# Optimization experiments

Measured on AMD Instinct MI355X. Metric: run time of the kernel, lower is better.

Reference implementation:

```python
import jax, jax.numpy as jnp
import numpy as np

F_DIM, HID, H, DQ, DV = 1024, 4096, 16, 64, 64
EPS = 1e-6

def layer_norm(x, w, b):
    mu = jnp.mean(x, axis=-1, keepdims=True)
    var = jnp.mean(jnp.square(x - mu), axis=-1, keepdims=True)
    return (x - mu) * jax.lax.rsqrt(var + EPS) * w + b

def setup_inputs() -> dict:
    key = jax.random.key(0)
    ks = jax.random.split(key, 8)
    s = 0.02
    return {
        'x': jax.random.normal(ks[0], (4, 2048, F_DIM), dtype=jnp.float32),
        'ln1_w': jnp.ones((F_DIM,), jnp.float32),
        'ln1_b': jnp.zeros((F_DIM,), jnp.float32),
        'wq_w': jax.random.normal(ks[1], (H * DQ, F_DIM), jnp.float32) * s,
        'wq_b': jnp.zeros((H * DQ,), jnp.float32),
        'wk_w': jax.random.normal(ks[2], (H * DQ, F_DIM), jnp.float32) * s,
        'wk_b': jnp.zeros((H * DQ,), jnp.float32),
        'wv_w': jax.random.normal(ks[3], (H * DV, F_DIM), jnp.float32) * s,
        'wv_b': jnp.zeros((H * DV,), jnp.float32),
        'fc_w': jax.random.normal(ks[4], (F_DIM, H * DV), jnp.float32) * s,
        'fc_b': jnp.zeros((F_DIM,), jnp.float32),
        'ln2_w': jnp.ones((F_DIM,), jnp.float32),
        'ln2_b': jnp.zeros((F_DIM,), jnp.float32),
        'fc1_w': jax.random.normal(ks[5], (HID, F_DIM), jnp.float32) * s,
        'fc1_b': jnp.zeros((HID,), jnp.float32),
        'fc2_w': jax.random.normal(ks[6], (F_DIM, HID), jnp.float32) * s,
        'fc2_b': jnp.zeros((F_DIM,), jnp.float32),
    }

def reference(x, ln1_w, ln1_b, wq_w, wq_b, wk_w, wk_b, wv_w, wv_b,
              fc_w, fc_b, ln2_w, ln2_b, fc1_w, fc1_b, fc2_w, fc2_b):
    B, S, _ = x.shape
    # --- pre-LN multi-head self-attention ---
    h = layer_norm(x, ln1_w, ln1_b)
    q = (h @ wq_w.T + wq_b).reshape(B, S, H, DQ).transpose(0, 2, 1, 3)  # [B,H,S,dq]
    k = (h @ wk_w.T + wk_b).reshape(B, S, H, DQ).transpose(0, 2, 1, 3)
    v = (h @ wv_w.T + wv_b).reshape(B, S, H, DV).transpose(0, 2, 1, 3)
    attn = jax.nn.softmax(jnp.einsum('bhqd,bhkd->bhqk', q, k) / jnp.sqrt(jnp.float32(DQ)), axis=-1)
    out = jnp.einsum('bhqk,bhkd->bhqd', attn, v).transpose(0, 2, 1, 3).reshape(B, S, H * DV)
    x = x + (out @ fc_w.T + fc_b)
    # --- pre-LN residual MLP ---
    h2 = layer_norm(x, ln2_w, ln2_b)
    ff = jax.nn.relu(h2 @ fc1_w.T + fc1_b) @ fc2_w.T + fc2_b
    return x + ff
```

## Files before the change

### kernel.cpp

```cpp
#include <hip/hip_runtime.h>

#define F_DIMC 1024
#define HIDC   4096
#define NH     16
#define SEQ    2048
#define BATCH  4
#define ROWS   (BATCH * SEQ)
#define MEG    (1u << 20)
#define QSCALE 0.18033688011112042f

typedef unsigned short u16t;
typedef __attribute__((ext_vector_type(8))) short short8;
typedef __attribute__((ext_vector_type(4))) float floatx4;
typedef __attribute__((address_space(1))) void gvoid_t;
typedef __attribute__((address_space(3))) void lvoid_t;
#define ASYNC16(g, l) __builtin_amdgcn_global_load_lds((gvoid_t*)(g), (lvoid_t*)(l), 16, 0, 0)

#if __has_builtin(__builtin_amdgcn_exp2f)
#define EXP2(x) __builtin_amdgcn_exp2f(x)
#else
#define EXP2(x) exp2f(x)
#endif

__device__ __forceinline__ u16t f2bf(float f) {
    union { float f; unsigned u; } v; v.f = f;
    unsigned r = v.u + 0x7fffu + ((v.u >> 16) & 1u);
    return (u16t)(r >> 16);
}
__device__ __forceinline__ unsigned fasu(float f) {
    union { float f; unsigned u; } v; v.f = f; return v.u;
}

__global__ __launch_bounds__(256) void ln_kernel(const float* __restrict__ x,
                                                 const float* __restrict__ w,
                                                 const float* __restrict__ b,
                                                 u16t* __restrict__ out) {
    const int row = blockIdx.x;
    const int t = threadIdx.x;
    const float* xp = x + (size_t)row * F_DIMC;

    float4 v = *(const float4*)(xp + t * 4);
    float s  = v.x + v.y + v.z + v.w;
    float ss = v.x * v.x + v.y * v.y + v.z * v.z + v.w * v.w;
    for (int off = 32; off; off >>= 1) {
        s  += __shfl_down(s, off);
        ss += __shfl_down(ss, off);
    }
    __shared__ float red[8];
    const int wid = t >> 6, lid = t & 63;
    if (lid == 0) { red[wid] = s; red[4 + wid] = ss; }
    __syncthreads();
    if (t == 0) {
        float S  = red[0] + red[1] + red[2] + red[3];
        float SS = red[4] + red[5] + red[6] + red[7];
        float mu  = S * (1.0f / F_DIMC);
        float var = SS * (1.0f / F_DIMC) - mu * mu;
        red[0] = mu;
        red[1] = rsqrtf(var + 1e-6f);
    }
    __syncthreads();
    const float mu = red[0], rs = red[1];

    float4 wv = *(const float4*)(w + t * 4);
    float4 bv = *(const float4*)(b + t * 4);
    ushort4 o = make_ushort4(f2bf((v.x - mu) * rs * wv.x + bv.x),
                             f2bf((v.y - mu) * rs * wv.y + bv.y),
                             f2bf((v.z - mu) * rs * wv.z + bv.z),
                             f2bf((v.w - mu) * rs * wv.w + bv.w));
    *(ushort4*)(out + (size_t)row * F_DIMC + t * 4) = o;
}

__global__ __launch_bounds__(256) void wconv_kernel(const float* __restrict__ w0,
        const float* __restrict__ w1, const float* __restrict__ w2,
        const float* __restrict__ w3, const float* __restrict__ w4,
        const float* __restrict__ w5, u16t* __restrict__ dst) {
    const size_t e = ((size_t)blockIdx.x * 256 + threadIdx.x) * 4;
    const float* src; size_t off;
    if      (e < 1 * MEG) { src = w0; off = e; }
    else if (e < 2 * MEG) { src = w1; off = e - 1 * MEG; }
    else if (e < 3 * MEG) { src = w2; off = e - 2 * MEG; }
    else if (e < 4 * MEG) { src = w3; off = e - 3 * MEG; }
    else if (e < 8 * MEG) { src = w4; off = e - 4 * MEG; }
    else                  { src = w5; off = e - 8 * MEG; }
    float4 f = *(const float4*)(src + off);
    *(ushort4*)(dst + e) = make_ushort4(f2bf(f.x), f2bf(f.y), f2bf(f.z), f2bf(f.w));
}

#define GEMM_PROLOGUE_AND_LOOP(Aq, Wq, Kdim)                                   \
    __shared__ u16t As[128 * 32] __attribute__((aligned(16)));                 \
    __shared__ u16t Ws[128 * 32] __attribute__((aligned(16)));                 \
    const int t = threadIdx.x;                                                 \
    const int lane = t & 63;                                                   \
    const int wave = t >> 6;                                                   \
    const int wm = wave >> 1, wn = wave & 1;                                   \
    const int m0 = blockIdx.y * 128, n0 = blockIdx.x * 128;                    \
    const int b0 = t, b1 = t + 256;                                            \
    const int r0 = b0 >> 2, r1 = b1 >> 2;                                      \
    const int q0_ = (b0 & 3) ^ (r0 & 3) ^ ((r0 >> 2) & 1);                     \
    const int q1_ = (b1 & 3) ^ (r1 & 3) ^ ((r1 >> 2) & 1);                     \
    const u16t* Ag0 = (Aq) + (size_t)(m0 + r0) * (Kdim) + q0_ * 8;             \
    const u16t* Ag1 = (Aq) + (size_t)(m0 + r1) * (Kdim) + q1_ * 8;             \
    const u16t* Wg0 = (Wq) + (size_t)(n0 + r0) * (Kdim) + q0_ * 8;             \
    const u16t* Wg1 = (Wq) + (size_t)(n0 + r1) * (Kdim) + q1_ * 8;             \
    u16t* Al0 = As + b0 * 8;  u16t* Al1 = As + b1 * 8;                         \
    u16t* Wl0 = Ws + b0 * 8;  u16t* Wl1 = Ws + b1 * 8;                         \
    const int fm = lane & 15, fq = lane >> 4;                                  \
    const int swz = fq ^ (fm & 3) ^ ((fm >> 2) & 1);                           \
    const u16t* Afp = As + ((wm * 64 + fm) * 32 + swz * 8);                    \
    const u16t* Wfp = Ws + ((wn * 64 + fm) * 32 + swz * 8);                    \
    floatx4 acc[4][4] = {};                                                    \
    for (int k0 = 0; k0 < (Kdim); k0 += 32) {                                  \
        ASYNC16(Ag0, Al0); ASYNC16(Ag1, Al1);                                  \
        ASYNC16(Wg0, Wl0); ASYNC16(Wg1, Wl1);                                  \
        Ag0 += 32; Ag1 += 32; Wg0 += 32; Wg1 += 32;                            \
        __syncthreads();                                                       \
        short8 fa[4], fb[4];                                                   \
        _Pragma("unroll")                                                      \
        for (int i = 0; i < 4; ++i) {                                          \
            fa[i] = *(const short8*)(Afp + i * 16 * 32);                       \
            fb[i] = *(const short8*)(Wfp + i * 16 * 32);                       \
        }                                                                      \
        _Pragma("unroll")                                                      \
        for (int mi = 0; mi < 4; ++mi)                                         \
            _Pragma("unroll")                                                  \
            for (int ni = 0; ni < 4; ++ni)                                     \
                acc[mi][ni] = __builtin_amdgcn_mfma_f32_16x16x32_bf16(         \
                    fa[mi], fb[ni], acc[mi][ni], 0, 0, 0);                     \
        __syncthreads();                                                       \
    }

template <bool RELU, bool RES, bool BF16OUT>
__global__ __launch_bounds__(256) void gemm_mfma(const u16t* __restrict__ A,
                                                 const u16t* __restrict__ W,
                                                 const float* __restrict__ bias,
                                                 const float* res, void* Cout,
                                                 int N, int K) {
    GEMM_PROLOGUE_AND_LOOP(A, W, K)
    float bl[4];
#pragma unroll
    for (int ni = 0; ni < 4; ++ni) bl[ni] = bias[n0 + wn * 64 + ni * 16 + fm];
#pragma unroll
    for (int mi = 0; mi < 4; ++mi) {
#pragma unroll
        for (int ni = 0; ni < 4; ++ni) {
            const int col = n0 + wn * 64 + ni * 16 + fm;
#pragma unroll
            for (int r = 0; r < 4; ++r) {
                const int row = m0 + wm * 64 + mi * 16 + fq * 4 + r;
                const size_t off = (size_t)row * N + col;
                float c = acc[mi][ni][r] + bl[ni];
                if (RELU) c = fmaxf(c, 0.0f);
                if (RES)  c += res[off];
                if (BF16OUT) ((u16t*)Cout)[off] = f2bf(c);
                else         ((float*)Cout)[off] = c;
            }
        }
    }
}

__global__ __launch_bounds__(256) void gemm_qkv(const u16t* __restrict__ A,
        const u16t* __restrict__ W,
        const float* __restrict__ wq_b, const float* __restrict__ wk_b,
        const float* __restrict__ wv_b,
        u16t* __restrict__ qb, u16t* __restrict__ kb, u16t* __restrict__ vtb) {
    GEMM_PROLOGUE_AND_LOOP(A, W, F_DIMC)
    const int which = n0 >> 10;
    const int nb = n0 & 1023;
    const float* bias = which == 0 ? wq_b : which == 1 ? wk_b : wv_b;
    float bl[4];
#pragma unroll
    for (int ni = 0; ni < 4; ++ni) bl[ni] = bias[nb + wn * 64 + ni * 16 + fm];

    if (which == 2) {
#pragma unroll
        for (int mi = 0; mi < 4; ++mi)
#pragma unroll
            for (int ni = 0; ni < 4; ++ni) {
                const int col = nb + wn * 64 + ni * 16 + fm;
                const int row0 = m0 + wm * 64 + mi * 16 + fq * 4;
                ushort4 pk = make_ushort4(f2bf(acc[mi][ni][0] + bl[ni]),
                                          f2bf(acc[mi][ni][1] + bl[ni]),
                                          f2bf(acc[mi][ni][2] + bl[ni]),
                                          f2bf(acc[mi][ni][3] + bl[ni]));
                *(ushort4*)(vtb + (size_t)col * ROWS + row0) = pk;
            }
    } else {
        u16t* dst = (which == 0) ? qb : kb;
        const float sc = (which == 0) ? QSCALE : 1.0f;
#pragma unroll
        for (int mi = 0; mi < 4; ++mi)
#pragma unroll
            for (int ni = 0; ni < 4; ++ni) {
                const int col = nb + wn * 64 + ni * 16 + fm;
#pragma unroll
                for (int r = 0; r < 4; ++r) {
                    const int row = m0 + wm * 64 + mi * 16 + fq * 4 + r;
                    dst[(size_t)row * F_DIMC + col] = f2bf((acc[mi][ni][r] + bl[ni]) * sc);
                }
            }
    }
}

__global__ __launch_bounds__(256, 4) void attn_mfma(const u16t* __restrict__ qb,
        const u16t* __restrict__ kbuf, const u16t* __restrict__ vtb,
        u16t* __restrict__ ab) {
    __shared__ u16t Kt[2][64 * 64] __attribute__((aligned(16)));
    __shared__ u16t Vs[64 * 64] __attribute__((aligned(16)));
    __shared__ u16t QP[128 * 64] __attribute__((aligned(16)));

    const int t = threadIdx.x;
    const int lane = t & 63;
    const int wave = t >> 6;
    const int l15 = lane & 15, q4 = lane >> 4;
    const int q0 = blockIdx.x * 128;
    const int bh = blockIdx.y;
    const int b = bh >> 4, hh = bh & 15;

#pragma unroll
    for (int c = 0; c < 4; ++c) {
        const int beta = c * 256 + t;
        const int r = beta >> 3, o = (beta & 7) ^ (r & 7);
        ASYNC16(qb + (size_t)(b * SEQ + q0 + r) * F_DIMC + hh * 64 + o * 8,
                QP + beta * 8);
    }
    const u16t* kg = kbuf + (size_t)(b * SEQ) * F_DIMC + hh * 64;
    const u16t* vg = vtb + (size_t)(hh * 64) * ROWS + b * SEQ;

    const int sb0 = t, sb1 = t + 256;
    const int sr0 = sb0 >> 3, so0 = (sb0 & 7) ^ (sr0 & 7);
    const int sr1 = sb1 >> 3, so1 = (sb1 & 7) ^ (sr1 & 7);
    const u16t* kp0 = kg + (size_t)sr0 * F_DIMC + so0 * 8;
    const u16t* kp1 = kg + (size_t)sr1 * F_DIMC + so1 * 8;
    const u16t* vp0 = vg + (size_t)sr0 * ROWS + so0 * 8;
    const u16t* vp1 = vg + (size_t)sr1 * ROWS + so1 * 8;

    ASYNC16(kp0, Kt[0] + sb0 * 8);
    ASYNC16(kp1, Kt[0] + sb1 * 8);
    ASYNC16(vp0, Vs + sb0 * 8);
    ASYNC16(vp1, Vs + sb1 * 8);
    kp0 += 64 * F_DIMC; kp1 += 64 * F_DIMC; vp0 += 64; vp1 += 64;
    __syncthreads();

    short8 fqr[2][2];
#pragma unroll
    for (int mt = 0; mt < 2; ++mt)
#pragma unroll
        for (int ks = 0; ks < 2; ++ks) {
            const int m = wave * 32 + mt * 16 + l15;
            const int oct = ks * 4 + q4;
            fqr[mt][ks] = *(const short8*)(QP + (m * 8 + (oct ^ (m & 7))) * 8);
        }

    short8 ones;
#pragma unroll
    for (int i = 0; i < 8; ++i) ones[i] = (short)0x3F80;

    floatx4 oacc[2][4] = {};
    floatx4 lacc[2] = {};

    for (int it = 0; it < SEQ / 64; ++it) {
        if (it + 1 < SEQ / 64) {
            u16t* kd = Kt[(it + 1) & 1];
            ASYNC16(kp0, kd + sb0 * 8);
            ASYNC16(kp1, kd + sb1 * 8);
            kp0 += 64 * F_DIMC; kp1 += 64 * F_DIMC;
        }
        const u16t* kcur = Kt[it & 1];

        short8 fk[4][2];
#pragma unroll
        for (int nt = 0; nt < 4; ++nt)
#pragma unroll
            for (int ks = 0; ks < 2; ++ks) {
                const int kr = nt * 16 + l15;
                const int oct = ks * 4 + q4;
                fk[nt][ks] = *(const short8*)(kcur + (kr * 8 + (oct ^ (kr & 7))) * 8);
            }
        floatx4 st[2][4] = {};
#pragma unroll
        for (int mt = 0; mt < 2; ++mt)
#pragma unroll
            for (int nt = 0; nt < 4; ++nt) {
                st[mt][nt] = __builtin_amdgcn_mfma_f32_16x16x32_bf16(
                    fk[nt][0], fqr[mt][0], st[mt][nt], 0, 0, 0);
                st[mt][nt] = __builtin_amdgcn_mfma_f32_16x16x32_bf16(
                    fk[nt][1], fqr[mt][1], st[mt][nt], 0, 0, 0);
            }

#pragma unroll
        for (int mt = 0; mt < 2; ++mt)
#pragma unroll
            for (int nt = 0; nt < 4; ++nt) {
                const float p0 = EXP2(st[mt][nt][0]);
                const float p1 = EXP2(st[mt][nt][1]);
                const float p2 = EXP2(st[mt][nt][2]);
                const float p3 = EXP2(st[mt][nt][3]);
                const unsigned lo = __builtin_amdgcn_perm(fasu(p1), fasu(p0), 0x07060302u);
                const unsigned hi = __builtin_amdgcn_perm(fasu(p3), fasu(p2), 0x07060302u);
                const int m = wave * 32 + mt * 16 + l15;
                const int logb = nt * 2 + (q4 >> 1);
                *(uint2*)(QP + (m * 8 + (logb ^ (m & 7))) * 8 + (q4 & 1) * 4) =
                    make_uint2(lo, hi);
            }

        __syncthreads();

        short8 fp[2][2], fv[4][2];
#pragma unroll
        for (int mt = 0; mt < 2; ++mt)
#pragma unroll
            for (int ks = 0; ks < 2; ++ks) {
                const int m = wave * 32 + mt * 16 + l15;
                const int oct = ks * 4 + q4;
                fp[mt][ks] = *(const short8*)(QP + (m * 8 + (oct ^ (m & 7))) * 8);
            }
#pragma unroll
        for (int nd = 0; nd < 4; ++nd)
#pragma unroll
            for (int ks = 0; ks < 2; ++ks) {
                const int d = nd * 16 + l15;
                const int oct = ks * 4 + q4;
                fv[nd][ks] = *(const short8*)(Vs + (d * 8 + (oct ^ (d & 7))) * 8);
            }
#pragma unroll
        for (int mt = 0; mt < 2; ++mt) {
#pragma unroll
            for (int nd = 0; nd < 4; ++nd) {
                oacc[mt][nd] = __builtin_amdgcn_mfma_f32_16x16x32_bf16(
                    fp[mt][0], fv[nd][0], oacc[mt][nd], 0, 0, 0);
                oacc[mt][nd] = __builtin_amdgcn_mfma_f32_16x16x32_bf16(
                    fp[mt][1], fv[nd][1], oacc[mt][nd], 0, 0, 0);
            }
            lacc[mt] = __builtin_amdgcn_mfma_f32_16x16x32_bf16(
                fp[mt][0], ones, lacc[mt], 0, 0, 0);
            lacc[mt] = __builtin_amdgcn_mfma_f32_16x16x32_bf16(
                fp[mt][1], ones, lacc[mt], 0, 0, 0);
        }

        __syncthreads();
        if (it + 1 < SEQ / 64) {
            ASYNC16(vp0, Vs + sb0 * 8);
            ASYNC16(vp1, Vs + sb1 * 8);
            vp0 += 64; vp1 += 64;
        }
    }

#pragma unroll
    for (int mt = 0; mt < 2; ++mt) {
        floatx4 rinv;
#pragma unroll
        for (int r = 0; r < 4; ++r) rinv[r] = 1.0f / lacc[mt][r];
#pragma unroll
        for (int nd = 0; nd < 4; ++nd)
#pragma unroll
            for (int r = 0; r < 4; ++r) {
                const int row = b * SEQ + q0 + wave * 32 + mt * 16 + q4 * 4 + r;
                const int col = hh * 64 + nd * 16 + l15;
                ab[(size_t)row * F_DIMC + col] = f2bf(oacc[mt][nd][r] * rinv[r]);
            }
    }
}

extern "C" void kernel_launch(void* const* d_in, const int* in_sizes, int n_in,
                              void* d_out, int out_size, void* d_ws, size_t ws_size,
                              hipStream_t stream) {
    const float* x     = (const float*)d_in[0];
    const float* ln1_w = (const float*)d_in[1];
    const float* ln1_b = (const float*)d_in[2];
    const float* wq_w  = (const float*)d_in[3];
    const float* wq_b  = (const float*)d_in[4];
    const float* wk_w  = (const float*)d_in[5];
    const float* wk_b  = (const float*)d_in[6];
    const float* wv_w  = (const float*)d_in[7];
    const float* wv_b  = (const float*)d_in[8];
    const float* fc_w  = (const float*)d_in[9];
    const float* fc_b  = (const float*)d_in[10];
    const float* ln2_w = (const float*)d_in[11];
    const float* ln2_b = (const float*)d_in[12];
    const float* fc1_w = (const float*)d_in[13];
    const float* fc1_b = (const float*)d_in[14];
    const float* fc2_w = (const float*)d_in[15];
    const float* fc2_b = (const float*)d_in[16];

    float* out = (float*)d_out;
    u16t*  ws  = (u16t*)d_ws;

    u16t* wbuf = ws;
    u16t* bwqkv = wbuf;
    u16t* bwfc = wbuf + 3 * MEG;
    u16t* bwf1 = wbuf + 4 * MEG;
    u16t* bwf2 = wbuf + 8 * MEG;
    u16t* h    = wbuf + 12 * MEG;
    u16t* qb   = h + 8 * MEG;
    u16t* kb   = qb + 8 * MEG;
    u16t* vtb  = kb + 8 * MEG;
    u16t* ab   = vtb + 8 * MEG;
    u16t* ff   = qb;

    const dim3 blk(256);
    const dim3 gF(F_DIMC / 128, ROWS / 128);
    const dim3 gQKV(3072 / 128, ROWS / 128);
    const dim3 gH(HIDC / 128, ROWS / 128);

    wconv_kernel<<<12 * MEG / 1024, blk, 0, stream>>>(wq_w, wk_w, wv_w, fc_w, fc1_w, fc2_w, wbuf);
    ln_kernel<<<ROWS, blk, 0, stream>>>(x, ln1_w, ln1_b, h);
    gemm_qkv<<<gQKV, blk, 0, stream>>>(h, bwqkv, wq_b, wk_b, wv_b, qb, kb, vtb);
    attn_mfma<<<dim3(SEQ / 128, BATCH * NH), blk, 0, stream>>>(qb, kb, vtb, ab);
    gemm_mfma<false, true, false><<<gF, blk, 0, stream>>>(ab, bwfc, fc_b, x, out, F_DIMC, F_DIMC);
    ln_kernel<<<ROWS, blk, 0, stream>>>(out, ln2_w, ln2_b, h);
    gemm_mfma<true, false, true><<<gH, blk, 0, stream>>>(h, bwf1, fc1_b, nullptr, ff, HIDC, F_DIMC);
    gemm_mfma<false, true, false><<<gF, blk, 0, stream>>>(ff, bwf2, fc2_b, out, out, F_DIMC, HIDC);
}
```

Before: 559.4 us.

## Split-K the fc2 GEMM with atomic accumulation and remap tiles for XCD locality

Adds a split-K variant of the fc2 GEMM that divides the 4096-long reduction into two halves along grid z. Each half atomically adds its partial sum into the residual output, and only the first half adds the bias. This doubles the block count of the long-K GEMM, which otherwise runs only 512 blocks for 4096 K-steps. It also changes every GEMM's block-to-tile mapping so that consecutive block IDs, which are spread across the 8 XCDs, cover contiguous M row ranges per XCD, aiming for better L2 reuse. The costs are float atomic traffic on the output, which also makes the summation order nondeterministic.

```diff
diff --git a/kernel.cpp b/kernel.cpp
--- a/kernel.cpp
+++ b/kernel.cpp
@@ -86,22 +86,26 @@
     *(ushort4*)(dst + e) = make_ushort4(f2bf(f.x), f2bf(f.y), f2bf(f.z), f2bf(f.w));
 }
 
-#define GEMM_PROLOGUE_AND_LOOP(Aq, Wq, Kdim)                                   \
+#define GEMM_PROLOGUE_AND_LOOP(Aq, Wq, Kdim, Kof, Klen)                        \
     __shared__ u16t As[128 * 32] __attribute__((aligned(16)));                 \
     __shared__ u16t Ws[128 * 32] __attribute__((aligned(16)));                 \
     const int t = threadIdx.x;                                                 \
     const int lane = t & 63;                                                   \
     const int wave = t >> 6;                                                   \
     const int wm = wave >> 1, wn = wave & 1;                                   \
-    const int m0 = blockIdx.y * 128, n0 = blockIdx.x * 128;                    \
+    const int l_ = blockIdx.y * gridDim.x + blockIdx.x;                        \
+    const int mper_ = gridDim.y >> 3;                                          \
+    const int r_ = l_ >> 3;                                                    \
+    const int m0 = ((l_ & 7) * mper_ + (r_ % mper_)) * 128;                    \
+    const int n0 = (r_ / mper_) * 128;                                         \
     const int b0 = t, b1 = t + 256;                                            \
     const int r0 = b0 >> 2, r1 = b1 >> 2;                                      \
     const int q0_ = (b0 & 3) ^ (r0 & 3) ^ ((r0 >> 2) & 1);                     \
     const int q1_ = (b1 & 3) ^ (r1 & 3) ^ ((r1 >> 2) & 1);                     \
-    const u16t* Ag0 = (Aq) + (size_t)(m0 + r0) * (Kdim) + q0_ * 8;             \
-    const u16t* Ag1 = (Aq) + (size_t)(m0 + r1) * (Kdim) + q1_ * 8;             \
-    const u16t* Wg0 = (Wq) + (size_t)(n0 + r0) * (Kdim) + q0_ * 8;             \
-    const u16t* Wg1 = (Wq) + (size_t)(n0 + r1) * (Kdim) + q1_ * 8;             \
+    const u16t* Ag0 = (Aq) + (size_t)(m0 + r0) * (Kdim) + (Kof) + q0_ * 8;     \
+    const u16t* Ag1 = (Aq) + (size_t)(m0 + r1) * (Kdim) + (Kof) + q1_ * 8;     \
+    const u16t* Wg0 = (Wq) + (size_t)(n0 + r0) * (Kdim) + (Kof) + q0_ * 8;     \
+    const u16t* Wg1 = (Wq) + (size_t)(n0 + r1) * (Kdim) + (Kof) + q1_ * 8;     \
     u16t* Al0 = As + b0 * 8;  u16t* Al1 = As + b1 * 8;                         \
     u16t* Wl0 = Ws + b0 * 8;  u16t* Wl1 = Ws + b1 * 8;                         \
     const int fm = lane & 15, fq = lane >> 4;                                  \
@@ -109,7 +113,7 @@
     const u16t* Afp = As + ((wm * 64 + fm) * 32 + swz * 8);                    \
     const u16t* Wfp = Ws + ((wn * 64 + fm) * 32 + swz * 8);                    \
     floatx4 acc[4][4] = {};                                                    \
-    for (int k0 = 0; k0 < (Kdim); k0 += 32) {                                  \
+    for (int k0 = 0; k0 < (Klen); k0 += 32) {                                  \
         ASYNC16(Ag0, Al0); ASYNC16(Ag1, Al1);                                  \
         ASYNC16(Wg0, Wl0); ASYNC16(Wg1, Wl1);                                  \
         Ag0 += 32; Ag1 += 32; Wg0 += 32; Wg1 += 32;                            \
@@ -135,7 +139,7 @@
                                                  const float* __restrict__ bias,
                                                  const float* res, void* Cout,
                                                  int N, int K) {
-    GEMM_PROLOGUE_AND_LOOP(A, W, K)
+    GEMM_PROLOGUE_AND_LOOP(A, W, K, 0, K)
     float bl[4];
 #pragma unroll
     for (int ni = 0; ni < 4; ++ni) bl[ni] = bias[n0 + wn * 64 + ni * 16 + fm];
@@ -158,12 +162,35 @@
     }
 }
 
+__global__ __launch_bounds__(256) void gemm_fc2(const u16t* __restrict__ A,
+                                                const u16t* __restrict__ W,
+                                                const float* __restrict__ bias,
+                                                float* __restrict__ out) {
+    const int kz = blockIdx.z;
+    GEMM_PROLOGUE_AND_LOOP(A, W, HIDC, kz * (HIDC / 2), HIDC / 2)
+    float bl[4];
+#pragma unroll
+    for (int ni = 0; ni < 4; ++ni)
+        bl[ni] = kz == 0 ? bias[n0 + wn * 64 + ni * 16 + fm] : 0.0f;
+#pragma unroll
+    for (int mi = 0; mi < 4; ++mi)
+#pragma unroll
+        for (int ni = 0; ni < 4; ++ni) {
+            const int col = n0 + wn * 64 + ni * 16 + fm;
+#pragma unroll
+            for (int r = 0; r < 4; ++r) {
+                const int row = m0 + wm * 64 + mi * 16 + fq * 4 + r;
+                atomicAdd(out + (size_t)row * F_DIMC + col, acc[mi][ni][r] + bl[ni]);
+            }
+        }
+}
+
 __global__ __launch_bounds__(256) void gemm_qkv(const u16t* __restrict__ A,
         const u16t* __restrict__ W,
         const float* __restrict__ wq_b, const float* __restrict__ wk_b,
         const float* __restrict__ wv_b,
         u16t* __restrict__ qb, u16t* __restrict__ kb, u16t* __restrict__ vtb) {
-    GEMM_PROLOGUE_AND_LOOP(A, W, F_DIMC)
+    GEMM_PROLOGUE_AND_LOOP(A, W, F_DIMC, 0, F_DIMC)
     const int which = n0 >> 10;
     const int nb = n0 & 1023;
     const float* bias = which == 0 ? wq_b : which == 1 ? wk_b : wv_b;
@@ -401,6 +428,7 @@
     const dim3 gF(F_DIMC / 128, ROWS / 128);
     const dim3 gQKV(3072 / 128, ROWS / 128);
     const dim3 gH(HIDC / 128, ROWS / 128);
+    const dim3 gF2(F_DIMC / 128, ROWS / 128, 2);
 
     wconv_kernel<<<12 * MEG / 1024, blk, 0, stream>>>(wq_w, wk_w, wv_w, fc_w, fc1_w, fc2_w, wbuf);
     ln_kernel<<<ROWS, blk, 0, stream>>>(x, ln1_w, ln1_b, h);
@@ -409,5 +437,5 @@
     gemm_mfma<false, true, false><<<gF, blk, 0, stream>>>(ab, bwfc, fc_b, x, out, F_DIMC, F_DIMC);
     ln_kernel<<<ROWS, blk, 0, stream>>>(out, ln2_w, ln2_b, h);
     gemm_mfma<true, false, true><<<gH, blk, 0, stream>>>(h, bwf1, fc1_b, nullptr, ff, HIDC, F_DIMC);
-    gemm_mfma<false, true, false><<<gF, blk, 0, stream>>>(ff, bwf2, fc2_b, out, out, F_DIMC, HIDC);
-}
+    gemm_fc2<<<gF2, blk, 0, stream>>>(ff, bwf2, fc2_b, out);
+}
```

New measurement: 574.6 us. 2.7% more time.
